# Performance work log

Measured on AMD Instinct MI355X. Metric: run time of the kernel, lower is better.

## Reference

```python
import jax, jax.numpy as jnp
import numpy as np

D_MODEL = 1024
NUM_HEAD = 16
D_K = D_MODEL // NUM_HEAD
B, S = 2, 2048


def setup_inputs() -> dict:
    key = jax.random.key(0)
    ks = jax.random.split(key, 12)
    s = 1.0 / np.sqrt(D_MODEL)
    return {
        "x_q": jax.random.normal(ks[0], (B, S, D_MODEL), jnp.float32),
        "x_k": jax.random.normal(ks[1], (B, S, D_MODEL), jnp.float32),
        "x_v": jax.random.normal(ks[2], (B, S, D_MODEL), jnp.float32),
        "mask": jax.random.randint(ks[3], (B, S, S), 0, 2, jnp.int32),
        "Wq": jax.random.uniform(ks[4], (D_MODEL, D_MODEL), jnp.float32, -s, s),
        "bq": jax.random.uniform(ks[5], (D_MODEL,), jnp.float32, -s, s),
        "Wk": jax.random.uniform(ks[6], (D_MODEL, D_MODEL), jnp.float32, -s, s),
        "bk": jax.random.uniform(ks[7], (D_MODEL,), jnp.float32, -s, s),
        "Wv": jax.random.uniform(ks[8], (D_MODEL, D_MODEL), jnp.float32, -s, s),
        "bv": jax.random.uniform(ks[9], (D_MODEL,), jnp.float32, -s, s),
        "Wo": jax.random.uniform(ks[10], (D_MODEL, D_MODEL), jnp.float32, -s, s),
        "bo": jax.random.uniform(ks[11], (D_MODEL,), jnp.float32, -s, s),
    }


def reference(x_q, x_k, x_v, mask, Wq, bq, Wk, bk, Wv, bv, Wo, bo):
    # projections -> [B, H, S, d_k]
    def proj(x, W, b):
        y = x @ W.T + b
        return y.reshape(B, -1, NUM_HEAD, D_K).transpose(0, 2, 1, 3)

    q = proj(x_q, Wq, bq)
    k = proj(x_k, Wk, bk)
    v = proj(x_v, Wv, bv)
    scale = 1.0 / np.sqrt(D_K).astype(np.float32)
    scores = jnp.einsum("bhqd,bhkd->bhqk", q, k) * scale
    scores = jnp.where(mask[:, None, :, :] == 0, jnp.float32(-1e9), scores)
    p = jax.nn.softmax(scores, axis=-1)  # dropout is identity in eval mode
    attn = jnp.einsum("bhqk,bhkd->bhqd", p, v)
    concat = attn.transpose(0, 2, 1, 3).reshape(B, S, D_MODEL)
    return concat @ Wo.T + bo
```

## Files before the change

kernel.cpp:

```cpp
#include <hip/hip_runtime.h>
#include <cstdint>
#include <cstddef>

#define D_MODELX 1024
#define NUM_HEADX 16
#define D_KX 64
#define BBX 2
#define SSX 2048
#define M_TOK 4096
#define MBYTE (1u << 20)

typedef __attribute__((ext_vector_type(8))) short short8;
typedef __attribute__((ext_vector_type(4))) short short4v;
typedef __attribute__((ext_vector_type(4))) float float4v;

__device__ __forceinline__ short f2bf(float f) {
  unsigned u = __builtin_bit_cast(unsigned, f);
  u = u + 0x7FFFu + ((u >> 16) & 1u);
  return (short)(u >> 16);
}

__global__ void mask_bits_kernel(const int* __restrict__ mask, unsigned* __restrict__ mbits) {
  int i = blockIdx.x * blockDim.x + threadIdx.x;
  bool v = mask[i] != 0;
  unsigned long long bal = __ballot(v);
  int lane = threadIdx.x & 63;
  if (lane == 0)       mbits[i >> 5] = (unsigned)bal;
  else if (lane == 32) mbits[i >> 5] = (unsigned)(bal >> 32);
}

__global__ void cvt_w4_kernel(const float* __restrict__ w0, const float* __restrict__ w1,
                              const float* __restrict__ w2, const float* __restrict__ w3,
                              short* __restrict__ o0, short* __restrict__ o1,
                              short* __restrict__ o2, short* __restrict__ o3) {
  int z = blockIdx.y;
  const float* in = (z == 0) ? w0 : (z == 1) ? w1 : (z == 2) ? w2 : w3;
  short* out = (z == 0) ? o0 : (z == 1) ? o1 : (z == 2) ? o2 : o3;
  int i = blockIdx.x * blockDim.x + threadIdx.x;
  float4v v = ((const float4v*)in)[i];
  short4v s;
  s[0] = f2bf(v[0]); s[1] = f2bf(v[1]); s[2] = f2bf(v[2]); s[3] = f2bf(v[3]);
  ((short4v*)out)[i] = s;
}

__global__ void cvt_x3_kernel(const float* __restrict__ x0, const float* __restrict__ x1,
                              const float* __restrict__ x2,
                              short* __restrict__ o0, short* __restrict__ o1,
                              short* __restrict__ o2) {
  int z = blockIdx.y;
  const float* in = (z == 0) ? x0 : (z == 1) ? x1 : x2;
  short* out = (z == 0) ? o0 : (z == 1) ? o1 : o2;
  int i = blockIdx.x * blockDim.x + threadIdx.x;
  float4v v = ((const float4v*)in)[i];
  short4v s;
  s[0] = f2bf(v[0]); s[1] = f2bf(v[1]); s[2] = f2bf(v[2]); s[3] = f2bf(v[3]);
  ((short4v*)out)[i] = s;
}

#define GBK 64

__device__ __forceinline__ void gemm_body(const short* __restrict__ A,
                                          const short* __restrict__ Bw,
                                          const float* __restrict__ bias,
                                          float oscale, void* __restrict__ outp, int mode) {
  __shared__ short lds_a[128 * 64];
  __shared__ short lds_b[128 * 64];
  const int tid = threadIdx.x;
  const int lane = tid & 63;
  const int wid = tid >> 6;
  const int wm = wid >> 1, wn = wid & 1;
  const int bn = blockIdx.x, bm = blockIdx.y;
  const int l15 = lane & 15, lg = lane >> 4;

  const int s_row = tid >> 3;
  const int s_cB = ((tid & 7) << 4) ^ ((s_row & 7) << 4);
  const short* Abase = A + (size_t)(bm * 128) * 1024 + (s_cB >> 1);
  const short* Bbase = Bw + (size_t)(bn * 128) * 1024 + (s_cB >> 1);

  const int xmask = (l15 & 7) << 4;
  const int a_b0 = (wm * 64 + l15) * 128 + ((lg * 16) ^ xmask);
  const int a_b1 = (wm * 64 + l15) * 128 + ((64 + lg * 16) ^ xmask);
  const int b_b0 = (wn * 64 + l15) * 128 + ((lg * 16) ^ xmask);
  const int b_b1 = (wn * 64 + l15) * 128 + ((64 + lg * 16) ^ xmask);

  float4v acc[4][4];
#pragma unroll
  for (int m = 0; m < 4; ++m)
#pragma unroll
    for (int n = 0; n < 4; ++n) acc[m][n] = (float4v){0.f, 0.f, 0.f, 0.f};

  for (int kt = 0; kt < 1024; kt += GBK) {
#pragma unroll
    for (int it = 0; it < 4; ++it) {
      int row = it * 32 + s_row;
      __builtin_amdgcn_global_load_lds(
          (const uint32_t*)(Abase + (size_t)row * 1024 + kt),
          (uint32_t*)(lds_a + (it * 256 + wid * 64) * 8), 16, 0, 0);
      __builtin_amdgcn_global_load_lds(
          (const uint32_t*)(Bbase + (size_t)row * 1024 + kt),
          (uint32_t*)(lds_b + (it * 256 + wid * 64) * 8), 16, 0, 0);
    }
    __syncthreads();

    short8 af[4][2];
#pragma unroll
    for (int m = 0; m < 4; ++m) {
      af[m][0] = *(const short8*)((const char*)lds_a + a_b0 + m * 2048);
      af[m][1] = *(const short8*)((const char*)lds_a + a_b1 + m * 2048);
    }
#pragma unroll
    for (int n = 0; n < 4; ++n) {
      short8 b0 = *(const short8*)((const char*)lds_b + b_b0 + n * 2048);
      short8 b1 = *(const short8*)((const char*)lds_b + b_b1 + n * 2048);
#pragma unroll
      for (int m = 0; m < 4; ++m) {
        acc[m][n] = __builtin_amdgcn_mfma_f32_16x16x32_bf16(af[m][0], b0, acc[m][n], 0, 0, 0);
        acc[m][n] = __builtin_amdgcn_mfma_f32_16x16x32_bf16(af[m][1], b1, acc[m][n], 0, 0, 0);
      }
    }
    __syncthreads();
  }

#pragma unroll
  for (int n = 0; n < 4; ++n) {
    int col = bn * 128 + wn * 64 + n * 16 + l15;
    float bv = bias[col];
#pragma unroll
    for (int m = 0; m < 4; ++m) {
      if (mode == 2) {
        int base_row = bm * 128 + wm * 64 + m * 16 + lg * 4;
        int bidx = base_row >> 11, s = base_row & 2047;
        int h = col >> 6, d = col & 63;
        short4v sv;
#pragma unroll
        for (int r = 0; r < 4; ++r) sv[r] = f2bf(acc[m][n][r] + bv);
        *(short4v*)&((short*)outp)[(((size_t)(bidx * NUM_HEADX + h)) * D_KX + d) * SSX + s] = sv;
      } else {
#pragma unroll
        for (int r = 0; r < 4; ++r) {
          int row = bm * 128 + wm * 64 + m * 16 + lg * 4 + r;
          float val = (acc[m][n][r] + bv) * oscale;
          if (mode == 0) {
            int bidx = row >> 11, s = row & 2047;
            int h = col >> 6, d = col & 63;
            ((short*)outp)[(((size_t)(bidx * NUM_HEADX + h)) * SSX + s) * D_KX + d] = f2bf(val);
          } else {
            ((float*)outp)[(size_t)row * D_MODELX + col] = val;
          }
        }
      }
    }
  }
}

__global__ __launch_bounds__(256) void gemm_qkv_kernel(
    const short* __restrict__ xq, const short* __restrict__ xk, const short* __restrict__ xv,
    const short* __restrict__ wq, const short* __restrict__ wk, const short* __restrict__ wv,
    const float* __restrict__ bq, const float* __restrict__ bk, const float* __restrict__ bv,
    short* __restrict__ qo, short* __restrict__ ko, short* __restrict__ vo, float qs) {
  int z = blockIdx.z;
  const short* A = (z == 0) ? xq : (z == 1) ? xk : xv;
  const short* W = (z == 0) ? wq : (z == 1) ? wk : wv;
  const float* bi = (z == 0) ? bq : (z == 1) ? bk : bv;
  void* out = (z == 0) ? (void*)qo : (z == 1) ? (void*)ko : (void*)vo;
  float os = (z == 0) ? qs : 1.0f;
  int mode = (z == 2) ? 2 : 0;
  gemm_body(A, W, bi, os, out, mode);
}

__global__ __launch_bounds__(256) void gemm_one_kernel(const short* __restrict__ A,
                                                       const short* __restrict__ W,
                                                       const float* __restrict__ bias,
                                                       float os, void* __restrict__ out, int mode) {
  gemm_body(A, W, bias, os, out, mode);
}

__global__ __launch_bounds__(256, 4) void attn_kernel(const short* __restrict__ q_ws,
                                                      const short* __restrict__ k_ws,
                                                      const short* __restrict__ vT_ws,
                                                      const unsigned* __restrict__ mbits,
                                                      short* __restrict__ attn_ws) {
  __shared__ short k_lds[2][64 * 64];
  __shared__ short vT_lds[2][64 * 64];
  __shared__ short p_lds[4][1024];

  const int tid = threadIdx.x;
  const int lane = tid & 63;
  const int w = tid >> 6;
  const int l15 = lane & 15, lg = lane >> 4;
  const int bid0 = blockIdx.x;
  const int bid = ((bid0 & 7) << 7) | (bid0 >> 3);
  const int qt = bid & 31;
  const int bh = bid >> 5;
  const int b = bh >> 4;
  const int h = bh & 15;

  const int qrow = qt * 64 + w * 16;

  const int xm15 = (l15 & 7) << 4;
  const int rd_c0 = l15 * 128 + ((lg * 16) ^ xm15);
  const int rd_c1 = l15 * 128 + ((64 + lg * 16) ^ xm15);
  char* kbase = (char*)k_lds;
  char* vbase = (char*)vT_lds;
  char* pwave = (char*)p_lds[w];
  const int pw_off = l15 * 32 + lg * 8;
  const int pr_off = (lg >> 1) * 512 + l15 * 32 + (lg & 1) * 16;

  const int srow = tid >> 2;
  const int scolS = (tid & 3) * 16;
  const int st0 = srow * 128 + ((scolS * 2) ^ ((srow & 7) << 4));
  const int st1 = srow * 128 + ((scolS * 2 + 16) ^ ((srow & 7) << 4));

  const short* kp = k_ws + (size_t)bh * SSX * D_KX + (size_t)srow * D_KX + scolS;
  const short* vp = vT_ws + (size_t)bh * D_KX * SSX + (size_t)srow * SSX + scolS;

  short8 qf[2];
#pragma unroll
  for (int f = 0; f < 2; ++f)
    qf[f] = *(const short8*)(q_ws + ((size_t)bh * SSX + qrow + l15) * D_KX + f * 32 + lg * 8);

  float4v acc[4];
#pragma unroll
  for (int db = 0; db < 4; ++db) acc[db] = (float4v){0.f, 0.f, 0.f, 0.f};
  float m_run = -INFINITY, l_part = 0.f;

  short8 kr0, kr1, vr0, vr1;
  auto loadt = [&](int kb) {
    const short* kq = kp + (size_t)kb * D_KX;
    kr0 = *(const short8*)kq;
    kr1 = *(const short8*)(kq + 8);
    const short* vq = vp + kb;
    vr0 = *(const short8*)vq;
    vr1 = *(const short8*)(vq + 8);
  };
  auto storet = [&](int BUF) {
    *(short8*)(kbase + BUF + st0) = kr0;
    *(short8*)(kbase + BUF + st1) = kr1;
    *(short8*)(vbase + BUF + st0) = vr0;
    *(short8*)(vbase + BUF + st1) = vr1;
  };

  const unsigned* mrow = mbits + ((size_t)b * SSX + qrow + l15) * (SSX / 32);
  unsigned long long mw = *(const unsigned long long*)mrow, mwn = 0;

  loadt(0);
  storet(0);
  loadt(64);
  __syncthreads();

  auto step = [&](int t, int CURB, int NXTB) {
    float p[4][4];
#pragma unroll
    for (int kf = 0; kf < 4; ++kf) {
      short8 k0 = *(const short8*)(kbase + CURB + rd_c0 + kf * 2048);
      short8 k1 = *(const short8*)(kbase + CURB + rd_c1 + kf * 2048);
      float4v f = (float4v){0.f, 0.f, 0.f, 0.f};
      f = __builtin_amdgcn_mfma_f32_16x16x32_bf16(k0, qf[0], f, 0, 0, 0);
      f = __builtin_amdgcn_mfma_f32_16x16x32_bf16(k1, qf[1], f, 0, 0, 0);
#pragma unroll
      for (int r = 0; r < 4; ++r) p[kf][r] = f[r];
    }

    if (t < 31) storet(NXTB);
    if (t < 30) loadt((t + 2) * 64);
    if (t < 31) mwn = *(const unsigned long long*)(mrow + 2 * (t + 1));

    float tmax = fmaxf(fmaxf(fmaxf(p[0][0], p[0][1]), fmaxf(p[0][2], p[0][3])),
                       fmaxf(fmaxf(p[1][0], p[1][1]), fmaxf(p[1][2], p[1][3])));
    tmax = fmaxf(tmax, fmaxf(fmaxf(fmaxf(p[2][0], p[2][1]), fmaxf(p[2][2], p[2][3])),
                             fmaxf(fmaxf(p[3][0], p[3][1]), fmaxf(p[3][2], p[3][3]))));
    if (!__all(tmax - m_run <= 8.0f)) {
      tmax = fmaxf(tmax, __shfl_xor(tmax, 16));
      tmax = fmaxf(tmax, __shfl_xor(tmax, 32));
      float mn = fmaxf(m_run, tmax);
      float corr = __builtin_amdgcn_exp2f(m_run - mn);
      m_run = mn;
      l_part *= corr;
#pragma unroll
      for (int db = 0; db < 4; ++db)
#pragma unroll
        for (int r = 0; r < 4; ++r) acc[db][r] *= corr;
    }

    unsigned long long sh = mw >> (lg * 4);
    unsigned mlo = (unsigned)sh, mhi = (unsigned)(sh >> 32);

    float tsum = 0.f;
#pragma unroll
    for (int kf = 0; kf < 4; ++kf) {
      float pv_[4];
#pragma unroll
      for (int r = 0; r < 4; ++r) {
        float pv = __builtin_amdgcn_exp2f(p[kf][r] - m_run);
        unsigned bit = (kf < 2 ? mlo : mhi) & (1u << ((kf & 1) * 16 + r));
        pv_[r] = bit ? pv : 0.0f;
      }
      tsum += (pv_[0] + pv_[1]) + (pv_[2] + pv_[3]);
      unsigned u0, u1;
      asm("v_cvt_pk_bf16_f32 %0, %1, %2" : "=v"(u0) : "v"(pv_[0]), "v"(pv_[1]));
      asm("v_cvt_pk_bf16_f32 %0, %1, %2" : "=v"(u1) : "v"(pv_[2]), "v"(pv_[3]));
      uint2 w2;
      w2.x = u0; w2.y = u1;
      *(uint2*)(pwave + pw_off + kf * 512) = w2;
    }
    l_part += tsum;

    short8 pa0 = *(const short8*)(pwave + pr_off);
    short8 pa1 = *(const short8*)(pwave + pr_off + 1024);

#pragma unroll
    for (int db = 0; db < 4; ++db) {
      short8 vb0 = *(const short8*)(vbase + CURB + rd_c0 + db * 2048);
      short8 vb1 = *(const short8*)(vbase + CURB + rd_c1 + db * 2048);
      acc[db] = __builtin_amdgcn_mfma_f32_16x16x32_bf16(vb0, pa0, acc[db], 0, 0, 0);
      acc[db] = __builtin_amdgcn_mfma_f32_16x16x32_bf16(vb1, pa1, acc[db], 0, 0, 0);
    }

    __syncthreads();
    mw = mwn;
  };

  for (int t2 = 0; t2 < 16; ++t2) {
    step(2 * t2, 0, 8192);
    step(2 * t2 + 1, 8192, 0);
  }

  l_part += __shfl_xor(l_part, 16);
  l_part += __shfl_xor(l_part, 32);
  float inv = 1.0f / l_part;

  size_t ttok = (size_t)b * SSX + qrow + l15;
#pragma unroll
  for (int db = 0; db < 4; ++db) {
    short4v sv;
#pragma unroll
    for (int r = 0; r < 4; ++r) sv[r] = f2bf(acc[db][r] * inv);
    *(short4v*)&attn_ws[ttok * D_MODELX + h * 64 + db * 16 + lg * 4] = sv;
  }
}

extern "C" void kernel_launch(void* const* d_in, const int* in_sizes, int n_in,
                              void* d_out, int out_size, void* d_ws, size_t ws_size,
                              hipStream_t stream) {
  const float* x_q = (const float*)d_in[0];
  const float* x_k = (const float*)d_in[1];
  const float* x_v = (const float*)d_in[2];
  const int*   mask = (const int*)d_in[3];
  const float* Wq = (const float*)d_in[4];
  const float* bq = (const float*)d_in[5];
  const float* Wk = (const float*)d_in[6];
  const float* bk = (const float*)d_in[7];
  const float* Wv = (const float*)d_in[8];
  const float* bv = (const float*)d_in[9];
  const float* Wo = (const float*)d_in[10];
  const float* bo = (const float*)d_in[11];

  const float QSCALE = 0.125f * 1.44269504089f;

  char* ws = (char*)d_ws;
  short* q_ws  = (short*)(ws + 0 * MBYTE);
  short* k_ws  = (short*)(ws + 8 * MBYTE);
  short* vT_ws = (short*)(ws + 16 * MBYTE);

  dim3 ggrid(D_MODELX / 128, M_TOK / 128);

  if (ws_size >= (size_t)56 * MBYTE) {
    short* wq_bf = (short*)(ws + 24 * MBYTE);
    short* wk_bf = (short*)(ws + 26 * MBYTE);
    short* wv_bf = (short*)(ws + 28 * MBYTE);
    short* wo_bf = (short*)(ws + 30 * MBYTE);
    short* xq_bf = (short*)(ws + 32 * MBYTE);
    short* xk_bf = (short*)(ws + 40 * MBYTE);
    short* xv_bf = (short*)(ws + 48 * MBYTE);
    short* attn_ws = (short*)(ws + 32 * MBYTE);
    unsigned* mbits = (unsigned*)(ws + 40 * MBYTE);

    cvt_w4_kernel<<<dim3(1024, 4), 256, 0, stream>>>(Wq, Wk, Wv, Wo, wq_bf, wk_bf, wv_bf, wo_bf);
    cvt_x3_kernel<<<dim3(4096, 3), 256, 0, stream>>>(x_q, x_k, x_v, xq_bf, xk_bf, xv_bf);

    dim3 qkvgrid(D_MODELX / 128, M_TOK / 128, 3);
    gemm_qkv_kernel<<<qkvgrid, 256, 0, stream>>>(xq_bf, xk_bf, xv_bf, wq_bf, wk_bf, wv_bf,
                                                 bq, bk, bv, q_ws, k_ws, vT_ws, QSCALE);

    mask_bits_kernel<<<(BBX * SSX * SSX) / 256, 256, 0, stream>>>(mask, mbits);

    attn_kernel<<<BBX * NUM_HEADX * (SSX / 64), 256, 0, stream>>>(q_ws, k_ws, vT_ws, mbits, attn_ws);

    gemm_one_kernel<<<ggrid, 256, 0, stream>>>(attn_ws, wo_bf, bo, 1.0f, d_out, 1);
  } else {
    unsigned* mbits = (unsigned*)(ws + 24 * MBYTE);
    short* w_bf = (short*)(ws + 25 * MBYTE);
    short* x_bf = (short*)(ws + 27 * MBYTE);
    short* attn_ws = (short*)(ws + 27 * MBYTE);

    mask_bits_kernel<<<(BBX * SSX * SSX) / 256, 256, 0, stream>>>(mask, mbits);

    cvt_w4_kernel<<<dim3(1024, 1), 256, 0, stream>>>(Wq, Wq, Wq, Wq, w_bf, w_bf, w_bf, w_bf);
    cvt_x3_kernel<<<dim3(4096, 1), 256, 0, stream>>>(x_q, x_q, x_q, x_bf, x_bf, x_bf);
    gemm_one_kernel<<<ggrid, 256, 0, stream>>>(x_bf, w_bf, bq, QSCALE, q_ws, 0);

    cvt_w4_kernel<<<dim3(1024, 1), 256, 0, stream>>>(Wk, Wk, Wk, Wk, w_bf, w_bf, w_bf, w_bf);
    cvt_x3_kernel<<<dim3(4096, 1), 256, 0, stream>>>(x_k, x_k, x_k, x_bf, x_bf, x_bf);
    gemm_one_kernel<<<ggrid, 256, 0, stream>>>(x_bf, w_bf, bk, 1.0f, k_ws, 0);

    cvt_w4_kernel<<<dim3(1024, 1), 256, 0, stream>>>(Wv, Wv, Wv, Wv, w_bf, w_bf, w_bf, w_bf);
    cvt_x3_kernel<<<dim3(4096, 1), 256, 0, stream>>>(x_v, x_v, x_v, x_bf, x_bf, x_bf);
    gemm_one_kernel<<<ggrid, 256, 0, stream>>>(x_bf, w_bf, bv, 1.0f, vT_ws, 2);

    attn_kernel<<<BBX * NUM_HEADX * (SSX / 64), 256, 0, stream>>>(q_ws, k_ws, vT_ws, mbits, attn_ws);

    cvt_w4_kernel<<<dim3(1024, 1), 256, 0, stream>>>(Wo, Wo, Wo, Wo, w_bf, w_bf, w_bf, w_bf);
    gemm_one_kernel<<<ggrid, 256, 0, stream>>>(attn_ws, w_bf, bo, 1.0f, d_out, 1);
  }
}
```

Measured before the change: 167.6 us.

## Double attention query tile per block to reuse K/V tiles across 32 rows per wave

```diff
diff --git a/kernel.cpp b/kernel.cpp
--- a/kernel.cpp
+++ b/kernel.cpp
@@ -13,6 +13,8 @@
 typedef __attribute__((ext_vector_type(8))) short short8;
 typedef __attribute__((ext_vector_type(4))) short short4v;
 typedef __attribute__((ext_vector_type(4))) float float4v;
+typedef __attribute__((ext_vector_type(2))) unsigned uint2v;
+typedef __attribute__((ext_vector_type(4))) unsigned uint4v;
 
 __device__ __forceinline__ short f2bf(float f) {
   unsigned u = __builtin_bit_cast(unsigned, f);
@@ -175,27 +177,27 @@
   gemm_body(A, W, bias, os, out, mode);
 }
 
-__global__ __launch_bounds__(256, 4) void attn_kernel(const short* __restrict__ q_ws,
+__global__ __launch_bounds__(256, 2) void attn_kernel(const short* __restrict__ q_ws,
                                                       const short* __restrict__ k_ws,
                                                       const short* __restrict__ vT_ws,
                                                       const unsigned* __restrict__ mbits,
                                                       short* __restrict__ attn_ws) {
-  __shared__ short k_lds[2][64 * 64];
-  __shared__ short vT_lds[2][64 * 64];
-  __shared__ short p_lds[4][1024];
+  __shared__ short k_lds[2][4096];
+  __shared__ short vT_lds[2][4096];
+  __shared__ short p_lds[4][2048];
 
   const int tid = threadIdx.x;
   const int lane = tid & 63;
   const int w = tid >> 6;
   const int l15 = lane & 15, lg = lane >> 4;
   const int bid0 = blockIdx.x;
-  const int bid = ((bid0 & 7) << 7) | (bid0 >> 3);
-  const int qt = bid & 31;
-  const int bh = bid >> 5;
+  const int bid = ((bid0 & 7) << 6) | (bid0 >> 3);
+  const int qt = bid & 15;
+  const int bh = bid >> 4;
   const int b = bh >> 4;
   const int h = bh & 15;
 
-  const int qrow = qt * 64 + w * 16;
+  const int qrow = qt * 128 + w * 32;
 
   const int xm15 = (l15 & 7) << 4;
   const int rd_c0 = l15 * 128 + ((lg * 16) ^ xm15);
@@ -203,8 +205,10 @@
   char* kbase = (char*)k_lds;
   char* vbase = (char*)vT_lds;
   char* pwave = (char*)p_lds[w];
-  const int pw_off = l15 * 32 + lg * 8;
-  const int pr_off = (lg >> 1) * 512 + l15 * 32 + (lg & 1) * 16;
+  const int s8 = ((l15 >> 2) & 3) << 3;
+  const int pw_off = l15 * 32 + ((lg * 8) ^ s8);
+  const int pr0 = (lg >> 1) * 512 + l15 * 32 + (((lg & 1) * 16) ^ s8);
+  const int pr1 = pr0 ^ 8;
 
   const int srow = tid >> 2;
   const int scolS = (tid & 3) * 16;
@@ -214,15 +218,20 @@
   const short* kp = k_ws + (size_t)bh * SSX * D_KX + (size_t)srow * D_KX + scolS;
   const short* vp = vT_ws + (size_t)bh * D_KX * SSX + (size_t)srow * SSX + scolS;
 
-  short8 qf[2];
-#pragma unroll
-  for (int f = 0; f < 2; ++f)
-    qf[f] = *(const short8*)(q_ws + ((size_t)bh * SSX + qrow + l15) * D_KX + f * 32 + lg * 8);
-
-  float4v acc[4];
-#pragma unroll
-  for (int db = 0; db < 4; ++db) acc[db] = (float4v){0.f, 0.f, 0.f, 0.f};
-  float m_run = -INFINITY, l_part = 0.f;
+  short8 qf[2][2];
+#pragma unroll
+  for (int qg = 0; qg < 2; ++qg)
+#pragma unroll
+    for (int c = 0; c < 2; ++c)
+      qf[qg][c] = *(const short8*)(q_ws + ((size_t)bh * SSX + qrow + qg * 16 + l15) * D_KX + c * 32 + lg * 8);
+
+  float4v acc[2][4];
+#pragma unroll
+  for (int qg = 0; qg < 2; ++qg)
+#pragma unroll
+    for (int db = 0; db < 4; ++db) acc[qg][db] = (float4v){0.f, 0.f, 0.f, 0.f};
+  float m_run[2] = {-INFINITY, -INFINITY};
+  float l_part[2] = {0.f, 0.f};
 
   short8 kr0, kr1, vr0, vr1;
   auto loadt = [&](int kb) {
@@ -240,8 +249,10 @@
     *(short8*)(vbase + BUF + st1) = vr1;
   };
 
-  const unsigned* mrow = mbits + ((size_t)b * SSX + qrow + l15) * (SSX / 32);
-  unsigned long long mw = *(const unsigned long long*)mrow, mwn = 0;
+  const unsigned* mrow0 = mbits + ((size_t)b * SSX + qrow + l15) * (SSX / 32);
+  const unsigned* mrow1 = mbits + ((size_t)b * SSX + qrow + 16 + l15) * (SSX / 32);
+  unsigned long long mw0 = *(const unsigned long long*)mrow0, mwn0 = 0;
+  unsigned long long mw1 = *(const unsigned long long*)mrow1, mwn1 = 0;
 
   loadt(0);
   storet(0);
@@ -249,75 +260,102 @@
   __syncthreads();
 
   auto step = [&](int t, int CURB, int NXTB) {
-    float p[4][4];
+    float p[2][4][4];
 #pragma unroll
     for (int kf = 0; kf < 4; ++kf) {
       short8 k0 = *(const short8*)(kbase + CURB + rd_c0 + kf * 2048);
       short8 k1 = *(const short8*)(kbase + CURB + rd_c1 + kf * 2048);
-      float4v f = (float4v){0.f, 0.f, 0.f, 0.f};
-      f = __builtin_amdgcn_mfma_f32_16x16x32_bf16(k0, qf[0], f, 0, 0, 0);
-      f = __builtin_amdgcn_mfma_f32_16x16x32_bf16(k1, qf[1], f, 0, 0, 0);
-#pragma unroll
-      for (int r = 0; r < 4; ++r) p[kf][r] = f[r];
+      float4v f0 = (float4v){0.f, 0.f, 0.f, 0.f};
+      f0 = __builtin_amdgcn_mfma_f32_16x16x32_bf16(k0, qf[0][0], f0, 0, 0, 0);
+      f0 = __builtin_amdgcn_mfma_f32_16x16x32_bf16(k1, qf[0][1], f0, 0, 0, 0);
+      float4v f1 = (float4v){0.f, 0.f, 0.f, 0.f};
+      f1 = __builtin_amdgcn_mfma_f32_16x16x32_bf16(k0, qf[1][0], f1, 0, 0, 0);
+      f1 = __builtin_amdgcn_mfma_f32_16x16x32_bf16(k1, qf[1][1], f1, 0, 0, 0);
+#pragma unroll
+      for (int r = 0; r < 4; ++r) { p[0][kf][r] = f0[r]; p[1][kf][r] = f1[r]; }
     }
 
     if (t < 31) storet(NXTB);
     if (t < 30) loadt((t + 2) * 64);
-    if (t < 31) mwn = *(const unsigned long long*)(mrow + 2 * (t + 1));
-
-    float tmax = fmaxf(fmaxf(fmaxf(p[0][0], p[0][1]), fmaxf(p[0][2], p[0][3])),
-                       fmaxf(fmaxf(p[1][0], p[1][1]), fmaxf(p[1][2], p[1][3])));
-    tmax = fmaxf(tmax, fmaxf(fmaxf(fmaxf(p[2][0], p[2][1]), fmaxf(p[2][2], p[2][3])),
-                             fmaxf(fmaxf(p[3][0], p[3][1]), fmaxf(p[3][2], p[3][3]))));
-    if (!__all(tmax - m_run <= 8.0f)) {
-      tmax = fmaxf(tmax, __shfl_xor(tmax, 16));
-      tmax = fmaxf(tmax, __shfl_xor(tmax, 32));
-      float mn = fmaxf(m_run, tmax);
-      float corr = __builtin_amdgcn_exp2f(m_run - mn);
-      m_run = mn;
-      l_part *= corr;
-#pragma unroll
-      for (int db = 0; db < 4; ++db)
-#pragma unroll
-        for (int r = 0; r < 4; ++r) acc[db][r] *= corr;
-    }
-
-    unsigned long long sh = mw >> (lg * 4);
-    unsigned mlo = (unsigned)sh, mhi = (unsigned)(sh >> 32);
-
-    float tsum = 0.f;
-#pragma unroll
-    for (int kf = 0; kf < 4; ++kf) {
-      float pv_[4];
-#pragma unroll
-      for (int r = 0; r < 4; ++r) {
-        float pv = __builtin_amdgcn_exp2f(p[kf][r] - m_run);
-        unsigned bit = (kf < 2 ? mlo : mhi) & (1u << ((kf & 1) * 16 + r));
-        pv_[r] = bit ? pv : 0.0f;
-      }
-      tsum += (pv_[0] + pv_[1]) + (pv_[2] + pv_[3]);
-      unsigned u0, u1;
-      asm("v_cvt_pk_bf16_f32 %0, %1, %2" : "=v"(u0) : "v"(pv_[0]), "v"(pv_[1]));
-      asm("v_cvt_pk_bf16_f32 %0, %1, %2" : "=v"(u1) : "v"(pv_[2]), "v"(pv_[3]));
-      uint2 w2;
-      w2.x = u0; w2.y = u1;
-      *(uint2*)(pwave + pw_off + kf * 512) = w2;
-    }
-    l_part += tsum;
-
-    short8 pa0 = *(const short8*)(pwave + pr_off);
-    short8 pa1 = *(const short8*)(pwave + pr_off + 1024);
+    if (t < 31) {
+      mwn0 = *(const unsigned long long*)(mrow0 + 2 * (t + 1));
+      mwn1 = *(const unsigned long long*)(mrow1 + 2 * (t + 1));
+    }
+
+    float tmax[2];
+#pragma unroll
+    for (int qg = 0; qg < 2; ++qg) {
+      float tm = fmaxf(fmaxf(fmaxf(p[qg][0][0], p[qg][0][1]), fmaxf(p[qg][0][2], p[qg][0][3])),
+                       fmaxf(fmaxf(p[qg][1][0], p[qg][1][1]), fmaxf(p[qg][1][2], p[qg][1][3])));
+      tm = fmaxf(tm, fmaxf(fmaxf(fmaxf(p[qg][2][0], p[qg][2][1]), fmaxf(p[qg][2][2], p[qg][2][3])),
+                           fmaxf(fmaxf(p[qg][3][0], p[qg][3][1]), fmaxf(p[qg][3][2], p[qg][3][3]))));
+      tmax[qg] = tm;
+    }
+    float dm = fmaxf(tmax[0] - m_run[0], tmax[1] - m_run[1]);
+    if (!__all(dm <= 8.0f)) {
+#pragma unroll
+      for (int qg = 0; qg < 2; ++qg) {
+        float tm = tmax[qg];
+        tm = fmaxf(tm, __shfl_xor(tm, 16));
+        tm = fmaxf(tm, __shfl_xor(tm, 32));
+        float mn = fmaxf(m_run[qg], tm);
+        float corr = __builtin_amdgcn_exp2f(m_run[qg] - mn);
+        m_run[qg] = mn;
+        l_part[qg] *= corr;
+#pragma unroll
+        for (int db = 0; db < 4; ++db)
+#pragma unroll
+          for (int r = 0; r < 4; ++r) acc[qg][db][r] *= corr;
+      }
+    }
+
+#pragma unroll
+    for (int qg = 0; qg < 2; ++qg) {
+      unsigned long long sh = (qg == 0 ? mw0 : mw1) >> (lg * 4);
+      unsigned mlo = (unsigned)sh, mhi = (unsigned)(sh >> 32);
+      float tsum = 0.f;
+#pragma unroll
+      for (int kf = 0; kf < 4; ++kf) {
+        float pv_[4];
+#pragma unroll
+        for (int r = 0; r < 4; ++r) {
+          float pv = __builtin_amdgcn_exp2f(p[qg][kf][r] - m_run[qg]);
+          unsigned bit = (kf < 2 ? mlo : mhi) & (1u << ((kf & 1) * 16 + r));
+          pv_[r] = bit ? pv : 0.0f;
+        }
+        tsum += (pv_[0] + pv_[1]) + (pv_[2] + pv_[3]);
+        unsigned u0, u1;
+        asm("v_cvt_pk_bf16_f32 %0, %1, %2" : "=v"(u0) : "v"(pv_[0]), "v"(pv_[1]));
+        asm("v_cvt_pk_bf16_f32 %0, %1, %2" : "=v"(u1) : "v"(pv_[2]), "v"(pv_[3]));
+        *(uint2v*)(pwave + pw_off + qg * 2048 + kf * 512) = (uint2v){u0, u1};
+      }
+      l_part[qg] += tsum;
+    }
+
+    short8 pa[2][2];
+#pragma unroll
+    for (int qg = 0; qg < 2; ++qg)
+#pragma unroll
+      for (int c = 0; c < 2; ++c) {
+        uint2v a0 = *(const uint2v*)(pwave + pr0 + qg * 2048 + c * 1024);
+        uint2v a1 = *(const uint2v*)(pwave + pr1 + qg * 2048 + c * 1024);
+        pa[qg][c] = __builtin_bit_cast(short8, (uint4v){a0[0], a0[1], a1[0], a1[1]});
+      }
 
 #pragma unroll
     for (int db = 0; db < 4; ++db) {
       short8 vb0 = *(const short8*)(vbase + CURB + rd_c0 + db * 2048);
       short8 vb1 = *(const short8*)(vbase + CURB + rd_c1 + db * 2048);
-      acc[db] = __builtin_amdgcn_mfma_f32_16x16x32_bf16(vb0, pa0, acc[db], 0, 0, 0);
-      acc[db] = __builtin_amdgcn_mfma_f32_16x16x32_bf16(vb1, pa1, acc[db], 0, 0, 0);
+#pragma unroll
+      for (int qg = 0; qg < 2; ++qg) {
+        acc[qg][db] = __builtin_amdgcn_mfma_f32_16x16x32_bf16(vb0, pa[qg][0], acc[qg][db], 0, 0, 0);
+        acc[qg][db] = __builtin_amdgcn_mfma_f32_16x16x32_bf16(vb1, pa[qg][1], acc[qg][db], 0, 0, 0);
+      }
     }
 
     __syncthreads();
-    mw = mwn;
+    mw0 = mwn0;
+    mw1 = mwn1;
   };
 
   for (int t2 = 0; t2 < 16; ++t2) {
@@ -325,17 +363,20 @@
     step(2 * t2 + 1, 8192, 0);
   }
 
-  l_part += __shfl_xor(l_part, 16);
-  l_part += __shfl_xor(l_part, 32);
-  float inv = 1.0f / l_part;
-
-  size_t ttok = (size_t)b * SSX + qrow + l15;
-#pragma unroll
-  for (int db = 0; db < 4; ++db) {
-    short4v sv;
-#pragma unroll
-    for (int r = 0; r < 4; ++r) sv[r] = f2bf(acc[db][r] * inv);
-    *(short4v*)&attn_ws[ttok * D_MODELX + h * 64 + db * 16 + lg * 4] = sv;
+#pragma unroll
+  for (int qg = 0; qg < 2; ++qg) {
+    float lp = l_part[qg];
+    lp += __shfl_xor(lp, 16);
+    lp += __shfl_xor(lp, 32);
+    float inv = 1.0f / lp;
+    size_t ttok = (size_t)b * SSX + qrow + qg * 16 + l15;
+#pragma unroll
+    for (int db = 0; db < 4; ++db) {
+      short4v sv;
+#pragma unroll
+      for (int r = 0; r < 4; ++r) sv[r] = f2bf(acc[qg][db][r] * inv);
+      *(short4v*)&attn_ws[ttok * D_MODELX + h * 64 + db * 16 + lg * 4] = sv;
+    }
   }
 }
 
@@ -384,7 +425,7 @@
 
     mask_bits_kernel<<<(BBX * SSX * SSX) / 256, 256, 0, stream>>>(mask, mbits);
 
-    attn_kernel<<<BBX * NUM_HEADX * (SSX / 64), 256, 0, stream>>>(q_ws, k_ws, vT_ws, mbits, attn_ws);
+    attn_kernel<<<BBX * NUM_HEADX * (SSX / 128), 256, 0, stream>>>(q_ws, k_ws, vT_ws, mbits, attn_ws);
 
     gemm_one_kernel<<<ggrid, 256, 0, stream>>>(attn_ws, wo_bf, bo, 1.0f, d_out, 1);
   } else {
@@ -407,7 +448,7 @@
     cvt_x3_kernel<<<dim3(4096, 1), 256, 0, stream>>>(x_v, x_v, x_v, x_bf, x_bf, x_bf);
     gemm_one_kernel<<<ggrid, 256, 0, stream>>>(x_bf, w_bf, bv, 1.0f, vT_ws, 2);
 
-    attn_kernel<<<BBX * NUM_HEADX * (SSX / 64), 256, 0, stream>>>(q_ws, k_ws, vT_ws, mbits, attn_ws);
+    attn_kernel<<<BBX * NUM_HEADX * (SSX / 128), 256, 0, stream>>>(q_ws, k_ws, vT_ws, mbits, attn_ws);
 
     cvt_w4_kernel<<<dim3(1024, 1), 256, 0, stream>>>(Wo, Wo, Wo, Wo, w_bf, w_bf, w_bf, w_bf);
     gemm_one_kernel<<<ggrid, 256, 0, stream>>>(attn_ws, w_bf, bo, 1.0f, d_out, 1);
```

New measurement: 168.0 us. About the same (+0.2%).
